# Optimization experiments

Measured on AMD Instinct MI355X. Metric: run time of the kernel, lower is better.

## Reference

```python
import jax, jax.numpy as jnp
import numpy as np

IFZ = 256      # in_features
SFZ = 1280     # sequence_features
AHZ = 8        # attention heads
AFZ = 64       # attention feature dim per head
NRES = 20      # canonical_num_residues
SCALE = float(np.sqrt(AFZ))
RESID = float(np.sqrt(2.0))
EPS = 1e-6


def _ln(x, s, b, eps=1e-5):
    m = jnp.mean(x, axis=-1, keepdims=True)
    v = jnp.var(x, axis=-1, keepdims=True)
    return (x - m) / jnp.sqrt(v + eps) * s + b


def setup_inputs() -> dict:
    key = jax.random.key(0)
    ks = jax.random.split(key, 20)
    N, B, S = 4096, 4, 512
    HD = AHZ * AFZ
    w = lambda k, shp: (jax.random.normal(k, shp, jnp.float32) * 0.02)
    d = {}
    d["x"] = jax.random.normal(ks[0], (N, IFZ), jnp.float32)
    d["packed_sequence_emb"] = jax.random.normal(ks[1], (B, S, SFZ), jnp.float32)
    d["packed_sequence_mask"] = jnp.ones((B, S), jnp.float32)
    d["prot_mask"] = jnp.arange(N, dtype=jnp.int32)
    d["batch"] = jax.random.randint(ks[2], (N,), 0, B, jnp.int32)
    # projections (bias=False)
    d["Wq"] = w(ks[3], (HD, IFZ))
    d["Wk"] = w(ks[4], (HD, SFZ))
    d["Wv"] = w(ks[5], (HD, SFZ))
    # ag: LayerNorm(HD) -> Linear(HD, IFZ, bias=False) (dropout = identity at eval)
    d["ag_ln_s"] = jnp.ones((HD,), jnp.float32)
    d["ag_ln_b"] = jnp.zeros((HD,), jnp.float32)
    d["Wag"] = w(ks[6], (IFZ, HD))
    d["res_ln_s"] = jnp.ones((3, IFZ), jnp.float32)
    d["res_ln_b"] = jnp.zeros((3, IFZ), jnp.float32)
    d["res_w1"] = w(ks[7], (3, IFZ, IFZ))
    d["res_b1"] = jnp.zeros((3, IFZ), jnp.float32)
    d["res_w2"] = w(ks[8], (3, IFZ, IFZ))
    d["res_b2"] = jnp.zeros((3, IFZ), jnp.float32)
    d["head_w"] = w(ks[9], (NRES, IFZ))
    d["head_b"] = jnp.zeros((NRES,), jnp.float32)
    # output LayerNorm en
    d["en_s"] = jnp.ones((IFZ,), jnp.float32)
    d["en_b"] = jnp.zeros((IFZ,), jnp.float32)
    return d


def _forward(x, emb, mask, prot_mask, batch, Wq, Wk, Wv, ag_ln_s, ag_ln_b, Wag,
             res_ln_s, res_ln_b, res_w1, res_b1, res_w2, res_b2,
             head_w, head_b, en_s, en_b):
    N = x.shape[0]
    B, S = emb.shape[:2]
    b_idx = batch[prot_mask]                      # [M]
    xp = x[prot_mask]                             # [M, IFZ]
    M = xp.shape[0]
    q = (xp @ Wq.T).reshape(M, AHZ, AFZ)          # [M,H,D]
    k = (emb @ Wk.T).reshape(B, S, AHZ, AFZ)      # [B,S,H,D]
    v = (emb @ Wv.T).reshape(B, S, AHZ, AFZ)
    # score vs every protein, then pick own protein (avoids materializing [M,S,H,D] gather)
    scores_all = jnp.einsum('mhd,bshd->mbsh', q, k) / SCALE          # [M,B,S,H]
    sel = b_idx[:, None, None, None]
    scores = jnp.take_along_axis(scores_all, sel, axis=1)[:, 0]       # [M,S,H]
    mb = mask[b_idx][:, :, None]                                      # [M,S,1]
    # padded_sequence_softmax: softmax over S, zero pads, renormalize
    sm = jax.nn.softmax(scores, axis=1) * mb
    w = sm / (jnp.sum(sm, axis=1, keepdims=True) + EPS)               # [M,S,H]
    feat_all = jnp.einsum('msh,bshd->mbhd', w, v)                     # [M,B,H,D]
    feat = jnp.take_along_axis(feat_all, sel, axis=1)[:, 0]
    feat = feat.reshape(M, AHZ * AFZ)
    ag = _ln(feat, ag_ln_s, ag_ln_b) @ Wag.T                          # [M, IFZ]
    # seq_aa_head on the scattered new features (identical to ag for unique prot_mask)
    h = ag
    for i in range(3):
        y = _ln(h, res_ln_s[i], res_ln_b[i])
        y = jax.nn.relu(y @ res_w1[i].T + res_b1[i])
        y = y @ res_w2[i].T + res_b2[i]
        h = (h + y) / RESID
    logits = h @ head_w.T + head_b                                     # [M, NRES]
    new_features = jnp.zeros_like(x).at[prot_mask].set(ag)
    seq_aa_logits = jnp.zeros((N, NRES), x.dtype).at[prot_mask].set(logits)
    unpacked_scores = jnp.zeros((N, S, AHZ), x.dtype).at[prot_mask].set(scores)
    out_x = _ln(x + new_features / RESID, en_s, en_b)
    return out_x, seq_aa_logits, unpacked_scores


def reference(x, packed_sequence_emb, packed_sequence_mask, prot_mask, batch,
              Wq, Wk, Wv, ag_ln_s, ag_ln_b, Wag,
              res_ln_s, res_ln_b, res_w1, res_b1, res_w2, res_b2,
              head_w, head_b, en_s, en_b):
    return _forward(x, packed_sequence_emb, packed_sequence_mask, prot_mask, batch,
                    Wq, Wk, Wv, ag_ln_s, ag_ln_b, Wag,
                    res_ln_s, res_ln_b, res_w1, res_b1, res_w2, res_b2,
                    head_w, head_b, en_s, en_b)
```

## Files before the change

### kernel.cpp

```cpp
#include <hip/hip_runtime.h>
#include <math.h>


typedef short bf8 __attribute__((ext_vector_type(8)));
typedef short bf4 __attribute__((ext_vector_type(4)));
typedef float f32x4 __attribute__((ext_vector_type(4)));
typedef unsigned short u16;

constexpr int LDT = 40;
enum { EPI_NONE = 0, EPI_BIAS_RELU = 1, EPI_BIAS = 2, EPI_RESID = 3 };
#define RSQRT2 0.70710678118654752f

__device__ __forceinline__ u16 f2bf(float f) {
  unsigned int u = __builtin_bit_cast(unsigned int, f);
  unsigned int r = u + 0x7fffu + ((u >> 16) & 1u);
  return (u16)(r >> 16);
}
__device__ __forceinline__ float bf2f(u16 v) {
  return __builtin_bit_cast(float, (unsigned int)v << 16);
}
__device__ __forceinline__ f32x4 mfma16(bf8 a, bf8 b, f32x4 c) {
  return __builtin_amdgcn_mfma_f32_16x16x32_bf16(a, b, c, 0, 0, 0);
}

struct CvtDesc { const float* src; u16* dst; int n; };
struct CvtArgs { CvtDesc d[8]; };

__global__ __launch_bounds__(256) void cvt_k(CvtArgs a) {
  CvtDesc d = a.d[blockIdx.z];
  int i = (blockIdx.x * 256 + threadIdx.x) * 8;
  if (i >= d.n) return;
  f32x4 v0 = *(const f32x4*)(d.src + i);
  f32x4 v1 = *(const f32x4*)(d.src + i + 4);
  bf8 o;
  o[0] = (short)f2bf(v0[0]); o[1] = (short)f2bf(v0[1]);
  o[2] = (short)f2bf(v0[2]); o[3] = (short)f2bf(v0[3]);
  o[4] = (short)f2bf(v1[0]); o[5] = (short)f2bf(v1[1]);
  o[6] = (short)f2bf(v1[2]); o[7] = (short)f2bf(v1[3]);
  *(bf8*)(d.dst + i) = o;
}

template <int EPI, bool BFOUT, int MT>
__global__ __launch_bounds__(256) void mgemm2(
    const u16* __restrict__ A, const u16* __restrict__ B,
    void* __restrict__ Cv, int M, int N, int K, int lda, int ldb, int ldc,
    const float* __restrict__ bias, const float* __restrict__ Hin,
    const int* __restrict__ gatherA, const int* __restrict__ scatterC) {
  constexpr int NF = MT / 32;
  __shared__ __align__(16) u16 As[MT * LDT];
  __shared__ __align__(16) u16 Bs[64 * LDT];
  const int tid = threadIdx.x;
  const int m0 = blockIdx.y * MT, n0 = blockIdx.x * 64;
  const int wave = tid >> 6, lane = tid & 63;
  const int wm = (wave & 1) * (MT / 2), wn = (wave >> 1) * 32;
  const int lrow = lane & 15, quad = lane >> 4;
  const int srow = tid >> 2, skq = tid & 3;

  int gr0 = m0 + srow;
  int ar0 = (gr0 < M) ? (gatherA ? gatherA[gr0] : gr0) : -1;
  const u16* Ap0 = (ar0 >= 0) ? A + (size_t)ar0 * lda + skq * 8 : nullptr;
  const u16* Ap1 = nullptr;
  if constexpr (MT == 128) {
    int gr1 = m0 + srow + 64;
    int ar1 = (gr1 < M) ? (gatherA ? gatherA[gr1] : gr1) : -1;
    Ap1 = (ar1 >= 0) ? A + (size_t)ar1 * lda + skq * 8 : nullptr;
  }
  const u16* Bp = (n0 + srow < N) ? B + (size_t)(n0 + srow) * ldb + skq * 8 : nullptr;
  u16* AsW0 = &As[srow * LDT + skq * 8];
  u16* AsW1 = (MT == 128) ? &As[(srow + 64) * LDT + skq * 8] : nullptr;
  u16* BsW = &Bs[srow * LDT + skq * 8];

  f32x4 acc[NF][2];
#pragma unroll
  for (int i = 0; i < NF; ++i)
#pragma unroll
    for (int j = 0; j < 2; ++j) acc[i][j] = (f32x4){0.f, 0.f, 0.f, 0.f};
  const bf8 z8 = {0, 0, 0, 0, 0, 0, 0, 0};

  for (int k0 = 0; k0 < K; k0 += 32) {
    bf8 a0 = Ap0 ? *(const bf8*)(Ap0 + k0) : z8;
    bf8 bv = Bp ? *(const bf8*)(Bp + k0) : z8;
    *(bf8*)AsW0 = a0;
    if constexpr (MT == 128) {
      bf8 a1 = Ap1 ? *(const bf8*)(Ap1 + k0) : z8;
      *(bf8*)AsW1 = a1;
    }
    *(bf8*)BsW = bv;
    __syncthreads();
    bf8 af[NF], bfr[2];
#pragma unroll
    for (int i = 0; i < NF; ++i)
      af[i] = *(const bf8*)&As[(wm + i * 16 + lrow) * LDT + quad * 8];
#pragma unroll
    for (int j = 0; j < 2; ++j)
      bfr[j] = *(const bf8*)&Bs[(wn + j * 16 + lrow) * LDT + quad * 8];
#pragma unroll
    for (int i = 0; i < NF; ++i)
#pragma unroll
      for (int j = 0; j < 2; ++j) acc[i][j] = mfma16(af[i], bfr[j], acc[i][j]);
    __syncthreads();
  }

  float* Cf = (float*)Cv;
  u16* Cb = (u16*)Cv;
#pragma unroll
  for (int i = 0; i < NF; ++i) {
#pragma unroll
    for (int r = 0; r < 4; ++r) {
      int row = m0 + wm + i * 16 + quad * 4 + r;
      if (row >= M) continue;
      if (gatherA && gatherA[row] < 0) continue;
      int orow = scatterC ? scatterC[row] : row;
#pragma unroll
      for (int j = 0; j < 2; ++j) {
        int col = n0 + wn + j * 16 + lrow;
        if (col >= N) continue;
        float v = acc[i][j][r];
        if (EPI == EPI_BIAS_RELU) v = fmaxf(v + bias[col], 0.f);
        else if (EPI == EPI_BIAS) v += bias[col];
        else if (EPI == EPI_RESID) v = (Hin[(size_t)row * ldc + col] + v + bias[col]) * RSQRT2;
        if (BFOUT) Cb[(size_t)orow * ldc + col] = f2bf(v);
        else Cf[(size_t)orow * ldc + col] = v;
      }
    }
  }
}

__global__ __launch_bounds__(256) void vtrans(const u16* __restrict__ KV,
                                              u16* __restrict__ VT) {
  __shared__ u16 t[32][33];
  int b = blockIdx.z;
  int s0 = blockIdx.x * 32, d0 = blockIdx.y * 32;
  int tx = threadIdx.x & 31, ty = threadIdx.x >> 5;
#pragma unroll
  for (int i = 0; i < 32; i += 8)
    t[ty + i][tx] = KV[(size_t)(b * 512 + s0 + ty + i) * 1024 + 512 + d0 + tx];
  __syncthreads();
#pragma unroll
  for (int i = 0; i < 32; i += 8)
    VT[(size_t)(b * 512 + d0 + ty + i) * 512 + s0 + tx] = t[tx][ty + i];
}

constexpr int WST = 520;
constexpr int QST = 72;

__global__ __launch_bounds__(256) void attn_fused(
    const u16* __restrict__ Q, const u16* __restrict__ KV,
    const u16* __restrict__ VT, const int* __restrict__ list,
    const float* __restrict__ mask, u16* __restrict__ packed,
    u16* __restrict__ feat, int N) {
  const int b = blockIdx.y >> 3, h = blockIdx.y & 7;
  const int mt = blockIdx.x;
  const int* lst = list + (size_t)b * N + mt * 32;
  if (lst[0] < 0) return;

  __shared__ __align__(16) u16 Ws[32 * WST];
  __shared__ __align__(16) u16 Qs[32 * QST];
  __shared__ __align__(16) u16 KVs[64 * QST];
  __shared__ __align__(16) float mk[8][68];
  __shared__ int mS[32];

  const int tid = threadIdx.x;
  const int wave = tid >> 6, lane = tid & 63;
  const int wm = (wave & 1) * 16, wns = (wave >> 1) * 32;
  const int lrow = lane & 15, quad = lane >> 4;
  const bf8 z8 = {0, 0, 0, 0, 0, 0, 0, 0};

  const int c0 = tid * 2, c1 = tid * 2 + 1;
  const int sr0 = c0 >> 3, kq0 = c0 & 7;
  const int sr1 = c1 >> 3, kq1 = c1 & 7;
  u16* kvw0 = &KVs[sr0 * QST + kq0 * 8];
  u16* kvw1 = &KVs[sr1 * QST + kq1 * 8];

  if (tid < 32) mS[tid] = lst[tid];
  {
    int p = tid >> 5, j = (tid & 31) * 2;
    *(float2*)&mk[p][j] = *(const float2*)&mask[(size_t)b * 512 + p * 64 + j];
  }
  {
    int qr = tid >> 3, kq = tid & 7;
    int m = lst[qr];
    *(bf8*)&Qs[qr * QST + kq * 8] =
        (m >= 0) ? *(const bf8*)(Q + (size_t)m * 512 + h * 64 + kq * 8) : z8;
  }
  const u16* KVb = KV + (size_t)(b * 512) * 1024 + h * 64;
  {
    int sta = mt & 7;
    *(bf8*)kvw0 = *(const bf8*)(KVb + (size_t)(sta * 64 + sr0) * 1024 + kq0 * 8);
    *(bf8*)kvw1 = *(const bf8*)(KVb + (size_t)(sta * 64 + sr1) * 1024 + kq1 * 8);
  }
  __syncthreads();

  const bf8 qa0 = *(const bf8*)&Qs[(wm + lrow) * QST + 0 + quad * 8];
  const bf8 qa1 = *(const bf8*)&Qs[(wm + lrow) * QST + 32 + quad * 8];

  bf8 r0, r1;
  for (int st = 0; st < 8; ++st) {
    const int sta = (st + mt) & 7;
    if (st < 7) {
      int nx = (st + 1 + mt) & 7;
      r0 = *(const bf8*)(KVb + (size_t)(nx * 64 + sr0) * 1024 + kq0 * 8);
      r1 = *(const bf8*)(KVb + (size_t)(nx * 64 + sr1) * 1024 + kq1 * 8);
    }
    f32x4 acc0 = {0.f, 0.f, 0.f, 0.f}, acc1 = acc0;
    {
      bf8 b00 = *(const bf8*)&KVs[(wns + lrow) * QST + quad * 8];
      bf8 b10 = *(const bf8*)&KVs[(wns + 16 + lrow) * QST + quad * 8];
      bf8 b01 = *(const bf8*)&KVs[(wns + lrow) * QST + 32 + quad * 8];
      bf8 b11 = *(const bf8*)&KVs[(wns + 16 + lrow) * QST + 32 + quad * 8];
      __builtin_amdgcn_s_setprio(1);
      acc0 = mfma16(qa0, b00, acc0);
      acc1 = mfma16(qa0, b10, acc1);
      acc0 = mfma16(qa1, b01, acc0);
      acc1 = mfma16(qa1, b11, acc1);
      __builtin_amdgcn_s_setprio(0);
    }
#pragma unroll
    for (int r = 0; r < 4; ++r) {
      int lr = wm + quad * 4 + r;
      Ws[lr * WST + sta * 64 + wns + lrow] = f2bf(acc0[r] * 0.125f);
      Ws[lr * WST + sta * 64 + wns + 16 + lrow] = f2bf(acc1[r] * 0.125f);
    }
    __syncthreads();
    if (st < 7) {
      *(bf8*)kvw0 = r0;
      *(bf8*)kvw1 = r1;
      __syncthreads();
    }
  }

  const u16* VTb = VT + (size_t)(b * 512 + h * 64) * 512;
  bf8 v0p = *(const bf8*)(VTb + (size_t)sr0 * 512 + ((mt & 7) << 6) + kq0 * 8);
  bf8 v1p = *(const bf8*)(VTb + (size_t)sr1 * 512 + ((mt & 7) << 6) + kq1 * 8);

  {
    const int row = tid >> 3, part = tid & 7;
    u16* wrow = &Ws[row * WST + part * 64];
    const int mm = mS[row];
    bf8 w[8];
    float mx = -1e30f;
#pragma unroll
    for (int v = 0; v < 8; ++v) {
      w[v] = *(const bf8*)(wrow + v * 8);
#pragma unroll
      for (int j = 0; j < 8; ++j) mx = fmaxf(mx, bf2f((u16)w[v][j]));
    }
    if (mm >= 0) {
      u16* prow = packed + ((size_t)h * N + mm) * 512 + part * 64;
#pragma unroll
      for (int v = 0; v < 8; ++v) *(bf8*)(prow + v * 8) = w[v];
    }
#pragma unroll
    for (int d = 1; d < 8; d <<= 1) mx = fmaxf(mx, __shfl_xor(mx, d));
    float ev[64];
    float se = 0.f, ms = 0.f;
#pragma unroll
    for (int v = 0; v < 8; ++v) {
      f32x4 m0 = *(const f32x4*)&mk[part][v * 8];
      f32x4 m1 = *(const f32x4*)&mk[part][v * 8 + 4];
#pragma unroll
      for (int j = 0; j < 8; ++j) {
        float e = __expf(bf2f((u16)w[v][j]) - mx);
        ev[v * 8 + j] = e;
        se += e;
        ms += e * (j < 4 ? m0[j] : m1[j - 4]);
      }
    }
#pragma unroll
    for (int d = 1; d < 8; d <<= 1) {
      se += __shfl_xor(se, d);
      ms += __shfl_xor(ms, d);
    }
    float iv = 1.0f / (ms + 1e-6f * se);
#pragma unroll
    for (int v = 0; v < 8; ++v) {
      f32x4 m0 = *(const f32x4*)&mk[part][v * 8];
      f32x4 m1 = *(const f32x4*)&mk[part][v * 8 + 4];
      bf8 o;
#pragma unroll
      for (int j = 0; j < 8; ++j)
        o[j] = (short)f2bf(ev[v * 8 + j] * (j < 4 ? m0[j] : m1[j - 4]) * iv);
      *(bf8*)(wrow + v * 8) = o;
    }
  }
  __syncthreads();
  *(bf8*)kvw0 = v0p;
  *(bf8*)kvw1 = v1p;
  __syncthreads();

  f32x4 acc0 = {0.f, 0.f, 0.f, 0.f}, acc1 = acc0;
  for (int ss = 0; ss < 8; ++ss) {
    const int s0 = ((ss + mt) & 7) << 6;
    if (ss < 7) {
      int nx = ((ss + 1 + mt) & 7) << 6;
      v0p = *(const bf8*)(VTb + (size_t)sr0 * 512 + nx + kq0 * 8);
      v1p = *(const bf8*)(VTb + (size_t)sr1 * 512 + nx + kq1 * 8);
    }
#pragma unroll
    for (int k0 = 0; k0 < 64; k0 += 32) {
      bf8 a = *(const bf8*)&Ws[(wm + lrow) * WST + s0 + k0 + quad * 8];
      bf8 b0 = *(const bf8*)&KVs[(wns + lrow) * QST + k0 + quad * 8];
      bf8 b1 = *(const bf8*)&KVs[(wns + 16 + lrow) * QST + k0 + quad * 8];
      __builtin_amdgcn_s_setprio(1);
      acc0 = mfma16(a, b0, acc0);
      acc1 = mfma16(a, b1, acc1);
      __builtin_amdgcn_s_setprio(0);
    }
    __syncthreads();
    if (ss < 7) {
      *(bf8*)kvw0 = v0p;
      *(bf8*)kvw1 = v1p;
      __syncthreads();
    }
  }
#pragma unroll
  for (int r = 0; r < 4; ++r) {
    int lr = wm + quad * 4 + r;
    int mm = mS[lr];
    if (mm < 0) continue;
    u16* frow = feat + (size_t)mm * 512 + h * 64;
    frow[wns + lrow] = f2bf(acc0[r]);
    frow[wns + 16 + lrow] = f2bf(acc1[r]);
  }
}

__global__ __launch_bounds__(256) void unpack_k(const u16* __restrict__ packed,
                                                const int* __restrict__ pm,
                                                float* __restrict__ out_sc,
                                                int N) {
  __shared__ u16 Ls[8 * 520];
  int m = blockIdx.x, tid = threadIdx.x;
  int h = tid >> 5, c = (tid & 31) * 16;
  const u16* row = packed + ((size_t)h * N + m) * 512 + c;
  *(bf8*)&Ls[h * 520 + c] = *(const bf8*)row;
  *(bf8*)&Ls[h * 520 + c + 8] = *(const bf8*)(row + 8);
  __syncthreads();
  float* orow = out_sc + (size_t)pm[m] * 4096;
#pragma unroll
  for (int i = 0; i < 16; ++i) {
    int e = tid + i * 256;
    orow[e] = bf2f(Ls[(e & 7) * 520 + (e >> 3)]);
  }
}

constexpr int HST = 268;
constexpr int AST = 520;
constexpr int YST = 280;

__global__ __launch_bounds__(1024) void mlp_fused(
    const u16* __restrict__ feat, const float* __restrict__ ag_s,
    const float* __restrict__ ag_b, const u16* __restrict__ Wag,
    const float* __restrict__ x, const float* __restrict__ ens,
    const float* __restrict__ enb, const float* __restrict__ rls,
    const float* __restrict__ rlb, const u16* __restrict__ rw1,
    const float* __restrict__ rb1, const u16* __restrict__ rw2,
    const float* __restrict__ rb2, const float* __restrict__ hw,
    const float* __restrict__ hb, const int* __restrict__ pm,
    float* __restrict__ out_lg, float* __restrict__ out_x) {
  __shared__ __align__(16) float Hs[16 * HST];
  __shared__ __align__(16) u16 As[16 * AST];
  __shared__ __align__(16) u16 Ys[16 * YST];
  const int tid = threadIdx.x;
  const int m0 = blockIdx.x * 16;
  const int wave = tid >> 6, lane = tid & 63;
  const int lrow = lane & 15, quad = lane >> 4;
  const int wn = wave * 16;
  const int row = wave;
  const int wq8 = quad * 8;
  const int nrow = pm[m0 + row];

  const u16* WagW = Wag + (size_t)(wn + lrow) * 512 + wq8;
  const u16* W1W = rw1 + (size_t)(wn + lrow) * 256 + wq8;
  const u16* W2W = rw2 + (size_t)(wn + lrow) * 256 + wq8;

  bf8 wp[8];
#pragma unroll
  for (int i = 0; i < 8; ++i) wp[i] = *(const bf8*)(WagW + i * 32);

  {
    const u16* frow = feat + (size_t)(m0 + row) * 512 + lane * 8;
    bf8 f0 = *(const bf8*)frow;
    float s = 0.f, sq = 0.f;
#pragma unroll
    for (int j = 0; j < 8; ++j) {
      float a = bf2f((u16)f0[j]);
      s += a;
      sq += a * a;
    }
#pragma unroll
    for (int d = 1; d < 64; d <<= 1) { s += __shfl_xor(s, d); sq += __shfl_xor(sq, d); }
    float mean = s * (1.0f / 512.0f);
    float var = sq * (1.0f / 512.0f) - mean * mean;
    float is = 1.0f / sqrtf(var + 1e-5f);
    int c = lane * 8;
    bf8 o0;
#pragma unroll
    for (int j = 0; j < 8; ++j)
      o0[j] = (short)f2bf((bf2f((u16)f0[j]) - mean) * is * ag_s[c + j] + ag_b[c + j]);
    *(bf8*)&As[row * AST + c] = o0;
  }
  __syncthreads();

  {
    f32x4 acc = {0.f, 0.f, 0.f, 0.f};
#pragma unroll
    for (int i = 0; i < 8; ++i) {
      bf8 a = *(const bf8*)&As[lrow * AST + i * 32 + wq8];
      acc = mfma16(a, wp[i], acc);
      wp[i] = *(const bf8*)(WagW + 256 + i * 32);
    }
#pragma unroll
    for (int i = 0; i < 8; ++i) {
      bf8 a = *(const bf8*)&As[lrow * AST + 256 + i * 32 + wq8];
      acc = mfma16(a, wp[i], acc);
      wp[i] = *(const bf8*)(W1W + i * 32);
    }
#pragma unroll
    for (int r = 0; r < 4; ++r) {
      int rr = quad * 4 + r;
      Hs[rr * HST + wn + lrow] = acc[r];
    }
  }
  __syncthreads();

  {
    int c = lane * 4;
    f32x4 xv = *(const f32x4*)&x[(size_t)nrow * 256 + c];
    f32x4 hv = *(const f32x4*)&Hs[row * HST + c];
    f32x4 v;
#pragma unroll
    for (int e = 0; e < 4; ++e) v[e] = xv[e] + hv[e] * RSQRT2;
    float s = v[0] + v[1] + v[2] + v[3];
    float sq = v[0] * v[0] + v[1] * v[1] + v[2] * v[2] + v[3] * v[3];
#pragma unroll
    for (int d = 1; d < 64; d <<= 1) { s += __shfl_xor(s, d); sq += __shfl_xor(sq, d); }
    float mean = s * (1.0f / 256.0f);
    float var = sq * (1.0f / 256.0f) - mean * mean;
    float is = 1.0f / sqrtf(var + 1e-5f);
    f32x4 o;
#pragma unroll
    for (int e = 0; e < 4; ++e)
      o[e] = (v[e] - mean) * is * ens[c + e] + enb[c + e];
    *(f32x4*)&out_x[(size_t)nrow * 256 + c] = o;
  }

  for (int layer = 0; layer < 3; ++layer) {
    {
      int c = lane * 4;
      f32x4 h0 = *(const f32x4*)&Hs[row * HST + c];
      float s = h0[0] + h0[1] + h0[2] + h0[3];
      float sq = h0[0] * h0[0] + h0[1] * h0[1] + h0[2] * h0[2] + h0[3] * h0[3];
#pragma unroll
      for (int d = 1; d < 64; d <<= 1) { s += __shfl_xor(s, d); sq += __shfl_xor(sq, d); }
      float mean = s * (1.0f / 256.0f);
      float var = sq * (1.0f / 256.0f) - mean * mean;
      float is = 1.0f / sqrtf(var + 1e-5f);
      const float* g = rls + layer * 256;
      const float* bb = rlb + layer * 256;
      bf4 o;
#pragma unroll
      for (int e = 0; e < 4; ++e)
        o[e] = (short)f2bf((h0[e] - mean) * is * g[c + e] + bb[c + e]);
      *(bf4*)&As[row * AST + c] = o;
    }
    __syncthreads();

    {
      f32x4 acc = {0.f, 0.f, 0.f, 0.f};
#pragma unroll
      for (int i = 0; i < 8; ++i) {
        bf8 a = *(const bf8*)&As[lrow * AST + i * 32 + wq8];
        acc = mfma16(a, wp[i], acc);
        wp[i] = *(const bf8*)(W2W + (size_t)layer * 65536 + i * 32);
      }
      float bi = rb1[layer * 256 + wn + lrow];
#pragma unroll
      for (int r = 0; r < 4; ++r) {
        int rr = quad * 4 + r;
        Ys[rr * YST + wn + lrow] = f2bf(fmaxf(acc[r] + bi, 0.f));
      }
    }
    __syncthreads();

    {
      f32x4 acc = {0.f, 0.f, 0.f, 0.f};
#pragma unroll
      for (int i = 0; i < 8; ++i) {
        bf8 a = *(const bf8*)&Ys[lrow * YST + i * 32 + wq8];
        acc = mfma16(a, wp[i], acc);
        if (layer < 2)
          wp[i] = *(const bf8*)(W1W + (size_t)(layer + 1) * 65536 + i * 32);
      }
      float bi = rb2[layer * 256 + wn + lrow];
#pragma unroll
      for (int r = 0; r < 4; ++r) {
        int rr = quad * 4 + r;
        float* h0 = &Hs[rr * HST + wn + lrow];
        *h0 = (*h0 + acc[r] + bi) * RSQRT2;
      }
    }
    __syncthreads();
  }

  if (lane < 20) {
    const float* hrow = &Hs[row * HST];
    const float* wrow = hw + (size_t)lane * 256;
    float l0 = 0.f, l1 = 0.f, l2 = 0.f, l3 = 0.f;
    for (int k = 0; k < 256; k += 16) {
      f32x4 h0 = *(const f32x4*)&hrow[k];
      f32x4 h1 = *(const f32x4*)&hrow[k + 4];
      f32x4 h2 = *(const f32x4*)&hrow[k + 8];
      f32x4 h3 = *(const f32x4*)&hrow[k + 12];
      f32x4 w0 = *(const f32x4*)&wrow[k];
      f32x4 w1 = *(const f32x4*)&wrow[k + 4];
      f32x4 w2 = *(const f32x4*)&wrow[k + 8];
      f32x4 w3 = *(const f32x4*)&wrow[k + 12];
#pragma unroll
      for (int e = 0; e < 4; ++e) {
        l0 += h0[e] * w0[e];
        l1 += h1[e] * w1[e];
        l2 += h2[e] * w2[e];
        l3 += h3[e] * w3[e];
      }
    }
    out_lg[(size_t)nrow * 20 + lane] = l0 + l1 + l2 + l3 + hb[lane];
  }
}

__global__ __launch_bounds__(256) void outx_k(
    const float* __restrict__ x, const int* __restrict__ inv,
    const float* __restrict__ g, const float* __restrict__ bb,
    float* __restrict__ out) {
  __shared__ float red[256];
  int n = blockIdx.x, tid = threadIdx.x;
  if (inv[n] >= 0) return;
  float v = x[(size_t)n * 256 + tid];
  red[tid] = v;
  __syncthreads();
  for (int off = 128; off; off >>= 1) {
    if (tid < off) red[tid] += red[tid + off];
    __syncthreads();
  }
  float mean = red[0] * (1.0f / 256.0f);
  __syncthreads();
  red[tid] = v * v;
  __syncthreads();
  for (int off = 128; off; off >>= 1) {
    if (tid < off) red[tid] += red[tid + off];
    __syncthreads();
  }
  float var = red[0] * (1.0f / 256.0f) - mean * mean;
  float is = 1.0f / sqrtf(var + 1e-5f);
  out[(size_t)n * 256 + tid] = (v - mean) * is * g[tid] + bb[tid];
}

__global__ void init_idx_k(int* __restrict__ list, int* __restrict__ inv,
                           int* __restrict__ cnt, int N, int B) {
  int i = blockIdx.x * 256 + threadIdx.x;
  if (i < B * N) list[i] = -1;
  if (i < N) inv[i] = -1;
  if (i < B) cnt[i] = 0;
}

__global__ void compact_k(const int* __restrict__ pm,
                          const int* __restrict__ batch, int* __restrict__ list,
                          int* __restrict__ inv, int* __restrict__ cnt, int N) {
  int m = blockIdx.x * 256 + threadIdx.x;
  if (m >= N) return;
  int p = pm[m];
  int b = batch[p];
  int slot = atomicAdd(&cnt[b], 1);
  list[(size_t)b * N + slot] = m;
  inv[p] = m;
}

extern "C" void kernel_launch(void* const* d_in, const int* in_sizes, int n_in,
                              void* d_out, int out_size, void* d_ws,
                              size_t ws_size, hipStream_t stream) {
  const float* x = (const float*)d_in[0];
  const float* emb = (const float*)d_in[1];
  const float* mask = (const float*)d_in[2];
  const int* pm = (const int*)d_in[3];
  const int* batch = (const int*)d_in[4];
  const float* Wq = (const float*)d_in[5];
  const float* Wk = (const float*)d_in[6];
  const float* Wv = (const float*)d_in[7];
  const float* ag_s = (const float*)d_in[8];
  const float* ag_b = (const float*)d_in[9];
  const float* Wag = (const float*)d_in[10];
  const float* rls = (const float*)d_in[11];
  const float* rlb = (const float*)d_in[12];
  const float* rw1 = (const float*)d_in[13];
  const float* rb1 = (const float*)d_in[14];
  const float* rw2 = (const float*)d_in[15];
  const float* rb2 = (const float*)d_in[16];
  const float* hw = (const float*)d_in[17];
  const float* hb = (const float*)d_in[18];
  const float* ens = (const float*)d_in[19];
  const float* enb = (const float*)d_in[20];

  const int N = in_sizes[0] / 256;
  const int B = in_sizes[2] / 512;

  char* wsb = (char*)d_ws;
  u16* embbf = (u16*)(wsb + 0);
  u16* xbf   = (u16*)(wsb + 5242880);
  u16* Wkvbf = (u16*)(wsb + 7340032);
  u16* Wqbf  = (u16*)(wsb + 9961472);
  u16* packed = (u16*)(wsb + 0);
  u16* KVbf   = (u16*)(wsb + 33554432);
  u16* Qbf    = (u16*)(wsb + 37748736);
  u16* VT     = (u16*)(wsb + 41943040);
  u16* featE  = (u16*)(wsb + 44040192);
  u16* Wagbf = (u16*)(wsb + 48234496);
  u16* rw1bf = (u16*)(wsb + 48496640);
  u16* rw2bf = (u16*)(wsb + 48889856);
  int* list  = (int*)(wsb + 49545216);
  int* inv   = (int*)(wsb + 49610752);
  int* cnt   = (int*)(wsb + 49627136);

  float* out_x = (float*)d_out;
  float* out_lg = out_x + (size_t)N * 256;
  float* out_sc = out_lg + (size_t)N * 20;

  CvtArgs ca;
  ca.d[0] = {emb, embbf, 2 * 512 * 1280 * 2};
  ca.d[1] = {x, xbf, 4096 * 256};
  ca.d[2] = {Wk, Wkvbf, 512 * 1280};
  ca.d[3] = {Wv, Wkvbf + 512 * 1280, 512 * 1280};
  ca.d[4] = {Wq, Wqbf, 512 * 256};
  ca.d[5] = {Wag, Wagbf, 256 * 512};
  ca.d[6] = {rw1, rw1bf, 3 * 256 * 256};
  ca.d[7] = {rw2, rw2bf, 3 * 256 * 256};
  cvt_k<<<dim3(1281, 1, 8), 256, 0, stream>>>(ca);
  init_idx_k<<<(B * N + 255) / 256, 256, 0, stream>>>(list, inv, cnt, N, B);
  compact_k<<<(N + 255) / 256, 256, 0, stream>>>(pm, batch, list, inv, cnt, N);

  mgemm2<EPI_NONE, true, 64><<<dim3(16, B * 8), 256, 0, stream>>>(
      embbf, Wkvbf, KVbf, B * 512, 1024, 1280, 1280, 1280, 1024,
      nullptr, nullptr, nullptr, nullptr);
  mgemm2<EPI_NONE, true, 64><<<dim3(8, N / 64), 256, 0, stream>>>(
      xbf, Wqbf, Qbf, N, 512, 256, 256, 256, 512,
      nullptr, nullptr, pm, nullptr);
  vtrans<<<dim3(16, 16, B), 256, 0, stream>>>(KVbf, VT);

  attn_fused<<<dim3(N / 32, B * 8), 256, 0, stream>>>(
      Qbf, KVbf, VT, list, mask, packed, featE, N);
  unpack_k<<<N, 256, 0, stream>>>(packed, pm, out_sc, N);

  mlp_fused<<<dim3(N / 16), 1024, 0, stream>>>(
      featE, ag_s, ag_b, Wagbf, x, ens, enb, rls, rlb, rw1bf, rb1,
      rw2bf, rb2, hw, hb, pm, out_lg, out_x);

  outx_k<<<N, 256, 0, stream>>>(x, inv, ens, enb, out_x);
}
```

Before: 288.3 us.

## Load K/V MFMA operands directly from global memory, dropping LDS staging and barriers

The attention kernel now loads the K and V^T MFMA B-operands directly from global memory into registers, software-prefetching one tile ahead. This removes the shared-memory staging buffers and the per-iteration __syncthreads. Q and the mask are likewise read straight from global memory, and the softmax recomputes the exponentials instead of holding a 64-entry register array. Launch bounds now request 4 blocks per CU. In exchange, the two waves that share an N-slice both fetch the same K/V data from global or cache, and the exp work is done twice.

Result: slower. 361.6 us (+25.4%).

```diff
diff --git a/kernel.cpp b/kernel.cpp
--- a/kernel.cpp
+++ b/kernel.cpp
@@ -142,9 +142,8 @@
 }
 
 constexpr int WST = 520;
-constexpr int QST = 72;
-
-__global__ __launch_bounds__(256) void attn_fused(
+
+__global__ __launch_bounds__(256, 4) void attn_fused(
     const u16* __restrict__ Q, const u16* __restrict__ KV,
     const u16* __restrict__ VT, const int* __restrict__ list,
     const float* __restrict__ mask, u16* __restrict__ packed,
@@ -155,9 +154,6 @@
   if (lst[0] < 0) return;
 
   __shared__ __align__(16) u16 Ws[32 * WST];
-  __shared__ __align__(16) u16 Qs[32 * QST];
-  __shared__ __align__(16) u16 KVs[64 * QST];
-  __shared__ __align__(16) float mk[8][68];
   __shared__ int mS[32];
 
   const int tid = threadIdx.x;
@@ -166,77 +162,65 @@
   const int lrow = lane & 15, quad = lane >> 4;
   const bf8 z8 = {0, 0, 0, 0, 0, 0, 0, 0};
 
-  const int c0 = tid * 2, c1 = tid * 2 + 1;
-  const int sr0 = c0 >> 3, kq0 = c0 & 7;
-  const int sr1 = c1 >> 3, kq1 = c1 & 7;
-  u16* kvw0 = &KVs[sr0 * QST + kq0 * 8];
-  u16* kvw1 = &KVs[sr1 * QST + kq1 * 8];
+  const u16* KVb = KV + (size_t)(b * 512) * 1024 + h * 64;
+  const u16* VTb = VT + (size_t)(b * 512 + h * 64) * 512;
+  const u16* K0 = KVb + (size_t)(wns + lrow) * 1024 + quad * 8;
+  const u16* K1 = KVb + (size_t)(wns + 16 + lrow) * 1024 + quad * 8;
+  const u16* V0 = VTb + (size_t)(wns + lrow) * 512 + quad * 8;
+  const u16* V1 = VTb + (size_t)(wns + 16 + lrow) * 512 + quad * 8;
+
+  const int st0 = (mt & 7) * 65536;
+  bf8 b00 = *(const bf8*)(K0 + st0);
+  bf8 b10 = *(const bf8*)(K1 + st0);
+  bf8 b01 = *(const bf8*)(K0 + st0 + 32);
+  bf8 b11 = *(const bf8*)(K1 + st0 + 32);
 
   if (tid < 32) mS[tid] = lst[tid];
-  {
-    int p = tid >> 5, j = (tid & 31) * 2;
-    *(float2*)&mk[p][j] = *(const float2*)&mask[(size_t)b * 512 + p * 64 + j];
-  }
-  {
-    int qr = tid >> 3, kq = tid & 7;
-    int m = lst[qr];
-    *(bf8*)&Qs[qr * QST + kq * 8] =
-        (m >= 0) ? *(const bf8*)(Q + (size_t)m * 512 + h * 64 + kq * 8) : z8;
-  }
-  const u16* KVb = KV + (size_t)(b * 512) * 1024 + h * 64;
-  {
-    int sta = mt & 7;
-    *(bf8*)kvw0 = *(const bf8*)(KVb + (size_t)(sta * 64 + sr0) * 1024 + kq0 * 8);
-    *(bf8*)kvw1 = *(const bf8*)(KVb + (size_t)(sta * 64 + sr1) * 1024 + kq1 * 8);
-  }
-  __syncthreads();
-
-  const bf8 qa0 = *(const bf8*)&Qs[(wm + lrow) * QST + 0 + quad * 8];
-  const bf8 qa1 = *(const bf8*)&Qs[(wm + lrow) * QST + 32 + quad * 8];
-
-  bf8 r0, r1;
+  __syncthreads();
+
+  const int qrow = mS[wm + lrow];
+  const u16* Qr = Q + (size_t)qrow * 512 + h * 64 + quad * 8;
+  const bf8 qa0 = (qrow >= 0) ? *(const bf8*)Qr : z8;
+  const bf8 qa1 = (qrow >= 0) ? *(const bf8*)(Qr + 32) : z8;
+
   for (int st = 0; st < 8; ++st) {
     const int sta = (st + mt) & 7;
+    bf8 n00, n10, n01, n11;
     if (st < 7) {
-      int nx = (st + 1 + mt) & 7;
-      r0 = *(const bf8*)(KVb + (size_t)(nx * 64 + sr0) * 1024 + kq0 * 8);
-      r1 = *(const bf8*)(KVb + (size_t)(nx * 64 + sr1) * 1024 + kq1 * 8);
+      const int nx = ((st + 1 + mt) & 7) * 65536;
+      n00 = *(const bf8*)(K0 + nx);
+      n10 = *(const bf8*)(K1 + nx);
+      n01 = *(const bf8*)(K0 + nx + 32);
+      n11 = *(const bf8*)(K1 + nx + 32);
     }
     f32x4 acc0 = {0.f, 0.f, 0.f, 0.f}, acc1 = acc0;
-    {
-      bf8 b00 = *(const bf8*)&KVs[(wns + lrow) * QST + quad * 8];
-      bf8 b10 = *(const bf8*)&KVs[(wns + 16 + lrow) * QST + quad * 8];
-      bf8 b01 = *(const bf8*)&KVs[(wns + lrow) * QST + 32 + quad * 8];
-      bf8 b11 = *(const bf8*)&KVs[(wns + 16 + lrow) * QST + 32 + quad * 8];
-      __builtin_amdgcn_s_setprio(1);
-      acc0 = mfma16(qa0, b00, acc0);
-      acc1 = mfma16(qa0, b10, acc1);
-      acc0 = mfma16(qa1, b01, acc0);
-      acc1 = mfma16(qa1, b11, acc1);
-      __builtin_amdgcn_s_setprio(0);
-    }
+    __builtin_amdgcn_s_setprio(1);
+    acc0 = mfma16(qa0, b00, acc0);
+    acc1 = mfma16(qa0, b10, acc1);
+    acc0 = mfma16(qa1, b01, acc0);
+    acc1 = mfma16(qa1, b11, acc1);
+    __builtin_amdgcn_s_setprio(0);
 #pragma unroll
     for (int r = 0; r < 4; ++r) {
       int lr = wm + quad * 4 + r;
       Ws[lr * WST + sta * 64 + wns + lrow] = f2bf(acc0[r] * 0.125f);
       Ws[lr * WST + sta * 64 + wns + 16 + lrow] = f2bf(acc1[r] * 0.125f);
     }
-    __syncthreads();
-    if (st < 7) {
-      *(bf8*)kvw0 = r0;
-      *(bf8*)kvw1 = r1;
-      __syncthreads();
-    }
-  }
-
-  const u16* VTb = VT + (size_t)(b * 512 + h * 64) * 512;
-  bf8 v0p = *(const bf8*)(VTb + (size_t)sr0 * 512 + ((mt & 7) << 6) + kq0 * 8);
-  bf8 v1p = *(const bf8*)(VTb + (size_t)sr1 * 512 + ((mt & 7) << 6) + kq1 * 8);
+    b00 = n00; b10 = n10; b01 = n01; b11 = n11;
+  }
+  __syncthreads();
+
+  const int sv0 = (mt & 7) << 6;
+  bf8 v00 = *(const bf8*)(V0 + sv0);
+  bf8 v10 = *(const bf8*)(V1 + sv0);
+  bf8 v01 = *(const bf8*)(V0 + sv0 + 32);
+  bf8 v11 = *(const bf8*)(V1 + sv0 + 32);
 
   {
     const int row = tid >> 3, part = tid & 7;
     u16* wrow = &Ws[row * WST + part * 64];
     const int mm = mS[row];
+    const float* mkp = mask + (size_t)b * 512 + part * 64;
     bf8 w[8];
     float mx = -1e30f;
 #pragma unroll
@@ -252,16 +236,14 @@
     }
 #pragma unroll
     for (int d = 1; d < 8; d <<= 1) mx = fmaxf(mx, __shfl_xor(mx, d));
-    float ev[64];
     float se = 0.f, ms = 0.f;
 #pragma unroll
     for (int v = 0; v < 8; ++v) {
-      f32x4 m0 = *(const f32x4*)&mk[part][v * 8];
-      f32x4 m1 = *(const f32x4*)&mk[part][v * 8 + 4];
+      f32x4 m0 = *(const f32x4*)(mkp + v * 8);
+      f32x4 m1 = *(const f32x4*)(mkp + v * 8 + 4);
 #pragma unroll
       for (int j = 0; j < 8; ++j) {
         float e = __expf(bf2f((u16)w[v][j]) - mx);
-        ev[v * 8 + j] = e;
         se += e;
         ms += e * (j < 4 ? m0[j] : m1[j - 4]);
       }
@@ -274,44 +256,39 @@
     float iv = 1.0f / (ms + 1e-6f * se);
 #pragma unroll
     for (int v = 0; v < 8; ++v) {
-      f32x4 m0 = *(const f32x4*)&mk[part][v * 8];
-      f32x4 m1 = *(const f32x4*)&mk[part][v * 8 + 4];
+      f32x4 m0 = *(const f32x4*)(mkp + v * 8);
+      f32x4 m1 = *(const f32x4*)(mkp + v * 8 + 4);
       bf8 o;
 #pragma unroll
-      for (int j = 0; j < 8; ++j)
-        o[j] = (short)f2bf(ev[v * 8 + j] * (j < 4 ? m0[j] : m1[j - 4]) * iv);
+      for (int j = 0; j < 8; ++j) {
+        float e = __expf(bf2f((u16)w[v][j]) - mx);
+        o[j] = (short)f2bf(e * (j < 4 ? m0[j] : m1[j - 4]) * iv);
+      }
       *(bf8*)(wrow + v * 8) = o;
     }
   }
-  __syncthreads();
-  *(bf8*)kvw0 = v0p;
-  *(bf8*)kvw1 = v1p;
   __syncthreads();
 
   f32x4 acc0 = {0.f, 0.f, 0.f, 0.f}, acc1 = acc0;
   for (int ss = 0; ss < 8; ++ss) {
     const int s0 = ((ss + mt) & 7) << 6;
+    bf8 nv00, nv10, nv01, nv11;
     if (ss < 7) {
-      int nx = ((ss + 1 + mt) & 7) << 6;
-      v0p = *(const bf8*)(VTb + (size_t)sr0 * 512 + nx + kq0 * 8);
-      v1p = *(const bf8*)(VTb + (size_t)sr1 * 512 + nx + kq1 * 8);
-    }
-#pragma unroll
-    for (int k0 = 0; k0 < 64; k0 += 32) {
-      bf8 a = *(const bf8*)&Ws[(wm + lrow) * WST + s0 + k0 + quad * 8];
-      bf8 b0 = *(const bf8*)&KVs[(wns + lrow) * QST + k0 + quad * 8];
-      bf8 b1 = *(const bf8*)&KVs[(wns + 16 + lrow) * QST + k0 + quad * 8];
-      __builtin_amdgcn_s_setprio(1);
-      acc0 = mfma16(a, b0, acc0);
-      acc1 = mfma16(a, b1, acc1);
-      __builtin_amdgcn_s_setprio(0);
-    }
-    __syncthreads();
-    if (ss < 7) {
-      *(bf8*)kvw0 = v0p;
-      *(bf8*)kvw1 = v1p;
-      __syncthreads();
-    }
+      const int nx = ((ss + 1 + mt) & 7) << 6;
+      nv00 = *(const bf8*)(V0 + nx);
+      nv10 = *(const bf8*)(V1 + nx);
+      nv01 = *(const bf8*)(V0 + nx + 32);
+      nv11 = *(const bf8*)(V1 + nx + 32);
+    }
+    bf8 a0 = *(const bf8*)&Ws[(wm + lrow) * WST + s0 + quad * 8];
+    bf8 a1 = *(const bf8*)&Ws[(wm + lrow) * WST + s0 + 32 + quad * 8];
+    __builtin_amdgcn_s_setprio(1);
+    acc0 = mfma16(a0, v00, acc0);
+    acc1 = mfma16(a0, v10, acc1);
+    acc0 = mfma16(a1, v01, acc0);
+    acc1 = mfma16(a1, v11, acc1);
+    __builtin_amdgcn_s_setprio(0);
+    v00 = nv00; v10 = nv10; v01 = nv01; v11 = nv11;
   }
 #pragma unroll
   for (int r = 0; r < 4; ++r) {
```
